# Kernel tuning notes

Hardware: AMD Instinct MI355X
Metric: run time of the kernel (lower is better)

## Reference

```python
import jax, jax.numpy as jnp
import numpy as np

N = 262144   # total atoms across all images
D = 128      # fingerprint (input_dimension)
H = 128      # hidden width (hiddenlayers = (128, 128))
S = 4        # number of unique element symbols (experts)
B = 1024     # number of images (segments)


def setup_inputs() -> dict:
    key = jax.random.key(0)
    ks = jax.random.split(key, 10)
    x = jax.random.normal(ks[0], (N, D), dtype=jnp.float32)
    symbol_ids = jax.random.randint(ks[1], (N,), 0, S, dtype=jnp.int32)
    image_ids = jnp.sort(jax.random.randint(ks[2], (N,), 0, B, dtype=jnp.int32))
    # per-symbol MLP params (xavier-ish scaling)
    W1 = jax.random.normal(ks[3], (S, D, H), dtype=jnp.float32) / np.sqrt(D)
    b1 = jnp.zeros((S, H), dtype=jnp.float32)
    W2 = jax.random.normal(ks[4], (S, H, H), dtype=jnp.float32) / np.sqrt(H)
    b2 = jnp.zeros((S, H), dtype=jnp.float32)
    W3 = jax.random.normal(ks[5], (S, H), dtype=jnp.float32) / np.sqrt(H)
    b3 = jnp.zeros((S,), dtype=jnp.float32)
    # per-symbol affine energy scale/shift
    slope = 1.0 + 0.1 * jax.random.normal(ks[6], (S,), dtype=jnp.float32)
    intercept = 0.1 * jax.random.normal(ks[7], (S,), dtype=jnp.float32)
    return {
        "x": x, "W1": W1, "b1": b1, "W2": W2, "b2": b2, "W3": W3, "b3": b3,
        "slope": slope, "intercept": intercept,
        "symbol_ids": symbol_ids, "image_ids": image_ids,
    }


def reference(x, W1, b1, W2, b2, W3, b3, slope, intercept, symbol_ids, image_ids):
    # Run every atom through every symbol's tiny MLP (S small), then select.
    h = jax.nn.relu(jnp.einsum('nd,sdh->nsh', x, W1) + b1)          # [N,S,H]
    h = jax.nn.relu(jnp.einsum('nsh,shk->nsk', h, W2) + b2)         # [N,S,H]
    e = jnp.einsum('nsh,sh->ns', h, W3) + b3                         # [N,S] atomic energy per expert
    e = slope * e + intercept                                        # per-symbol affine
    e_atom = jnp.take_along_axis(e, symbol_ids[:, None].astype(jnp.int32), axis=1)[:, 0]  # [N] routed
    # per-image energy = sum of atomic energies in that image
    return jax.ops.segment_sum(e_atom, image_ids, num_segments=B)    # [B]
```

## Files before the change

kernel.cpp:

```cpp
#include <hip/hip_runtime.h>
#include <hip/hip_bf16.h>
#include <stdint.h>

typedef _Float16 f16x8 __attribute__((ext_vector_type(8)));
typedef __fp16 hf2 __attribute__((ext_vector_type(2)));
typedef float f32x4 __attribute__((ext_vector_type(4)));
typedef unsigned int u32x4 __attribute__((ext_vector_type(4)));
typedef unsigned int u32x2 __attribute__((ext_vector_type(2)));

#define N_ATOMS 262144
#define NSYM 4
#define NIMG 1024

__global__ void hist_kernel(const int* __restrict__ sym, int* __restrict__ wbh) {
  int b = blockIdx.x;
  int i = b * 256 + threadIdx.x;
  int lane = threadIdx.x & 63, wave = threadIdx.x >> 6;
  __shared__ int wcnt[4][NSYM];
  int s = sym[i];
#pragma unroll
  for (int t = 0; t < NSYM; ++t) {
    unsigned long long m = __ballot(s == t);
    if (lane == 0) wcnt[wave][t] = __popcll(m);
  }
  __syncthreads();
  if (threadIdx.x < NSYM)
    wbh[b * 4 + threadIdx.x] = wcnt[0][threadIdx.x] + wcnt[1][threadIdx.x] +
                               wcnt[2][threadIdx.x] + wcnt[3][threadIdx.x];
}

__global__ void offsets_kernel(const int* __restrict__ wbh, int* __restrict__ bases,
                               int* __restrict__ offs, int* __restrict__ perm) {
  __shared__ int wtot[4][NSYM];
  __shared__ int offsh[NSYM + 1];
  __shared__ int totsh[NSYM];
  int t = threadIdx.x, lane = t & 63, wave = t >> 6;
  int pre[4][NSYM];
  int sum[NSYM] = {0, 0, 0, 0};
#pragma unroll
  for (int k = 0; k < 4; ++k)
#pragma unroll
    for (int s2 = 0; s2 < NSYM; ++s2) {
      pre[k][s2] = sum[s2];
      sum[s2] += wbh[(t * 4 + k) * 4 + s2];
    }
  int inc[NSYM] = {sum[0], sum[1], sum[2], sum[3]};
  for (int d = 1; d < 64; d <<= 1) {
#pragma unroll
    for (int s2 = 0; s2 < NSYM; ++s2) {
      int v = __shfl_up(inc[s2], d);
      if (lane >= d) inc[s2] += v;
    }
  }
  if (lane == 63)
#pragma unroll
    for (int s2 = 0; s2 < NSYM; ++s2) wtot[wave][s2] = inc[s2];
  __syncthreads();
  int wb[NSYM];
#pragma unroll
  for (int s2 = 0; s2 < NSYM; ++s2) {
    wb[s2] = 0;
    for (int w = 0; w < wave; ++w) wb[s2] += wtot[w][s2];
  }
  if (t == 255)
#pragma unroll
    for (int s2 = 0; s2 < NSYM; ++s2) totsh[s2] = wb[s2] + inc[s2];
  __syncthreads();
  if (t == 0) {
    int o = 0;
    offsh[0] = 0; offs[0] = 0;
    for (int s2 = 0; s2 < NSYM; ++s2) {
      o += (totsh[s2] + 255) & ~255;
      offsh[s2 + 1] = o; offs[s2 + 1] = o;
    }
  }
  __syncthreads();
#pragma unroll
  for (int k = 0; k < 4; ++k)
#pragma unroll
    for (int s2 = 0; s2 < NSYM; ++s2)
      bases[(t * 4 + k) * 4 + s2] = offsh[s2] + wb[s2] + (inc[s2] - sum[s2]) + pre[k][s2];
  for (int s2 = 0; s2 < NSYM; ++s2) {
    int lo = offsh[s2] + totsh[s2], hi = offsh[s2 + 1];
    for (int i = lo + t; i < hi; i += 256) perm[i] = -1;
  }
}

__global__ void scatter_kernel(const int* __restrict__ sym, const int* __restrict__ bases,
                               int* __restrict__ perm) {
  int b = blockIdx.x;
  int i = b * 256 + threadIdx.x;
  int lane = threadIdx.x & 63, wave = threadIdx.x >> 6;
  __shared__ int wcnt[4][NSYM];
  int s = sym[i];
  unsigned long long mymask = 0;
#pragma unroll
  for (int t = 0; t < NSYM; ++t) {
    unsigned long long m = __ballot(s == t);
    if (lane == 0) wcnt[wave][t] = __popcll(m);
    if (s == t) mymask = m;
  }
  __syncthreads();
  int off = bases[b * 4 + s];
  for (int w = 0; w < wave; ++w) off += wcnt[w][s];
  off += __popcll(mymask & ((1ull << lane) - 1ull));
  perm[off] = i;
}

__global__ void wconv_kernel(const float* __restrict__ W1, const float* __restrict__ W2,
                             unsigned short* __restrict__ wt) {
  int idx = blockIdx.x * 256 + threadIdx.x;
  int t = idx >> 14;
  int layer = t >> 2, s = t & 3;
  int rem = idx & 16383;
  int h = rem >> 7, u = rem & 127;
  int gs = u >> 3, j = u & 7;
  int d = ((gs ^ (h & 7)) << 3) + j;
  const float* W = layer ? W2 : W1;
  _Float16 hv = (_Float16)W[(s * 128 + d) * 128 + h];
  wt[t * 16384 + h * 128 + u] = __builtin_bit_cast(unsigned short, hv);
}

__global__ __launch_bounds__(512, 2) void mlp_gemm(
    const float* __restrict__ x, const unsigned short* __restrict__ wt,
    const int* __restrict__ perm, const int* __restrict__ offs,
    const float* __restrict__ b1, const float* __restrict__ b2,
    const float* __restrict__ W3, const float* __restrict__ b3,
    const float* __restrict__ slope, const float* __restrict__ intercept,
    float* __restrict__ e_atom) {
  extern __shared__ char lds[];

  int s = blockIdx.x >> 6;
  int kblk = blockIdx.x & 63;
  int base = offs[s];
  int T = (offs[s + 1] - base) >> 8;

  int tid = threadIdx.x;
  int wave = tid >> 6, lane = tid & 63;
  int r0 = lane & 15, chunk = lane >> 4;
  int l32 = lane & 31, half = lane >> 5;
  char* stage = lds + 65536 + wave * 8192;

  const unsigned short* w1p = wt + (size_t)(0 + s) * 16384;
  const unsigned short* w2p = wt + (size_t)(4 + s) * 16384;

#pragma unroll
  for (int it = 0; it < 8; ++it) {
    int gb = it * 512 + wave * 64;
    const unsigned short* src = (gb >= 2048) ? (w2p + (size_t)(gb - 2048 + lane) * 8)
                                             : (w1p + (size_t)(gb + lane) * 8);
    __builtin_amdgcn_global_load_lds((const unsigned int*)src,
                                     (unsigned int*)(lds + (size_t)gb * 16), 16, 0, 0);
  }

  float b1v[8], b2v[8], w3v[8];
#pragma unroll
  for (int cf = 0; cf < 8; ++cf) {
    b1v[cf] = b1[s * 128 + cf * 16 + r0];
    b2v[cf] = b2[s * 128 + cf * 16 + r0];
    w3v[cf] = W3[s * 128 + cf * 16 + r0];
  }
  float sl = slope[s], ic = intercept[s], bb = b3[s];

  int cur_perm = (kblk < T) ? perm[base + (kblk << 8) + wave * 32 + l32] : -1;
  float4 raw[16];
#pragma unroll
  for (int it = 0; it < 16; ++it) {
    int atom = __shfl(cur_perm, it * 2 + half);
    raw[it] = *(const float4*)(x + (size_t)(atom < 0 ? 0 : atom) * 128 + l32 * 4);
  }

  __syncthreads();

  f32x4 zero4 = {0.f, 0.f, 0.f, 0.f};

  for (int t = kblk; t < T; t += 64) {
    int tn = t + 64;
    int nperm = -1;
    if (tn < T) nperm = perm[base + (tn << 8) + wave * 32 + l32];

#pragma unroll
    for (int it = 0; it < 16; ++it) {
      int row = it * 2 + half;
      hf2 p0 = __builtin_amdgcn_cvt_pkrtz(raw[it].x, raw[it].y);
      hf2 p1 = __builtin_amdgcn_cvt_pkrtz(raw[it].z, raw[it].w);
      u32x2 w2 = {__builtin_bit_cast(unsigned int, p0), __builtin_bit_cast(unsigned int, p1)};
      int gs = (l32 >> 1) ^ (row & 7);
      *(u32x2*)(stage + row * 256 + gs * 16 + (l32 & 1) * 8) = w2;
    }
    f16x8 ah[8];
#pragma unroll
    for (int rf = 0; rf < 2; ++rf)
#pragma unroll
      for (int kk = 0; kk < 4; ++kk) {
        int row = rf * 16 + r0;
        ah[rf * 4 + kk] = *(const f16x8*)(stage + row * 256 +
                                          (((kk * 4 + chunk) ^ (row & 7)) << 4));
      }

    f32x4 acc[2][8];
#pragma unroll
    for (int i = 0; i < 2; ++i)
#pragma unroll
      for (int j = 0; j < 8; ++j) acc[i][j] = zero4;

#pragma unroll
    for (int k = 0; k < 4; ++k)
#pragma unroll
      for (int cf = 0; cf < 8; ++cf) {
        int row = cf * 16 + r0;
        f16x8 bh = *(const f16x8*)(lds + row * 256 +
                                   ((((k * 4 + chunk)) << 4) ^ ((row & 7) << 4)));
        acc[0][cf] = __builtin_amdgcn_mfma_f32_16x16x32_f16(ah[k], bh, acc[0][cf], 0, 0, 0);
        acc[1][cf] = __builtin_amdgcn_mfma_f32_16x16x32_f16(ah[4 + k], bh, acc[1][cf], 0, 0, 0);
      }

#pragma unroll
    for (int hp2 = 0; hp2 < 2; ++hp2) {
#pragma unroll
      for (int cf4 = 0; cf4 < 4; ++cf4) {
        int cf = hp2 * 4 + cf4;
        float bias = b1v[cf];
        int colp = cf4 * 16 + r0;
#pragma unroll
        for (int rf = 0; rf < 2; ++rf)
#pragma unroll
          for (int rr = 0; rr < 4; ++rr) {
            int row = rf * 16 + chunk * 4 + rr;
            float v = fmaxf(acc[rf][cf][rr] + bias, 0.f);
            unsigned short h = __builtin_bit_cast(unsigned short, (_Float16)v);
            int cc = colp ^ (chunk << 4) ^ (rr << 2);
            *(unsigned int*)(stage + row * 256 + cc * 4) = ((unsigned int)h << 16) | h;
          }
      }
#pragma unroll
      for (int kk2 = 0; kk2 < 2; ++kk2) {
        int kk = hp2 * 2 + kk2;
#pragma unroll
        for (int rf = 0; rf < 2; ++rf) {
          int row = rf * 16 + r0;
          int xr3 = ((r0 >> 2) << 4) ^ ((r0 & 3) << 2);
          int c0 = kk2 * 32 + chunk * 8;
          u32x4 pa = *(const u32x4*)(stage + row * 256 + (c0 ^ xr3) * 4);
          u32x4 pb = *(const u32x4*)(stage + row * 256 + ((c0 + 4) ^ xr3) * 4);
          unsigned int h01 = (pa[0] >> 16) | (pa[1] & 0xffff0000u);
          unsigned int h23 = (pa[2] >> 16) | (pa[3] & 0xffff0000u);
          unsigned int h45 = (pb[0] >> 16) | (pb[1] & 0xffff0000u);
          unsigned int h67 = (pb[2] >> 16) | (pb[3] & 0xffff0000u);
          u32x4 hq = {h01, h23, h45, h67};
          ah[rf * 4 + kk] = __builtin_bit_cast(f16x8, hq);
        }
      }
    }

    if (tn < T) {
#pragma unroll
      for (int it = 0; it < 16; ++it) {
        int atom = __shfl(nperm, it * 2 + half);
        raw[it] = *(const float4*)(x + (size_t)(atom < 0 ? 0 : atom) * 128 + l32 * 4);
      }
    }

#pragma unroll
    for (int i = 0; i < 2; ++i)
#pragma unroll
      for (int j = 0; j < 8; ++j) acc[i][j] = zero4;

#pragma unroll
    for (int k = 0; k < 4; ++k)
#pragma unroll
      for (int cf = 0; cf < 8; ++cf) {
        int row = cf * 16 + r0;
        f16x8 bh = *(const f16x8*)(lds + 32768 + row * 256 +
                                   ((((k * 4 + chunk)) << 4) ^ ((row & 7) << 4)));
        acc[0][cf] = __builtin_amdgcn_mfma_f32_16x16x32_f16(ah[k], bh, acc[0][cf], 0, 0, 0);
        acc[1][cf] = __builtin_amdgcn_mfma_f32_16x16x32_f16(ah[4 + k], bh, acc[1][cf], 0, 0, 0);
      }

    float p[2][4] = {{0.f, 0.f, 0.f, 0.f}, {0.f, 0.f, 0.f, 0.f}};
#pragma unroll
    for (int cf = 0; cf < 8; ++cf)
#pragma unroll
      for (int rf = 0; rf < 2; ++rf)
#pragma unroll
        for (int rr = 0; rr < 4; ++rr)
          p[rf][rr] += fmaxf(acc[rf][cf][rr] + b2v[cf], 0.f) * w3v[cf];
#pragma unroll
    for (int m = 1; m < 16; m <<= 1)
#pragma unroll
      for (int rf = 0; rf < 2; ++rf)
#pragma unroll
        for (int rr = 0; rr < 4; ++rr) p[rf][rr] += __shfl_xor(p[rf][rr], m);

    int atom_w[2][4];
#pragma unroll
    for (int rf = 0; rf < 2; ++rf)
#pragma unroll
      for (int rr = 0; rr < 4; ++rr)
        atom_w[rf][rr] = __shfl(cur_perm, rf * 16 + chunk * 4 + rr);

    if (r0 == 0) {
#pragma unroll
      for (int rf = 0; rf < 2; ++rf)
#pragma unroll
        for (int rr = 0; rr < 4; ++rr)
          if (atom_w[rf][rr] >= 0)
            e_atom[atom_w[rf][rr]] = sl * (p[rf][rr] + bb) + ic;
    }

    cur_perm = nperm;
  }
}

__global__ void segsum_kernel(const float* __restrict__ e_atom, const int* __restrict__ img,
                              float* __restrict__ out, int n) {
  int b = blockIdx.x;
  int lo = 0, hi = n;
  while (lo < hi) { int m = (lo + hi) >> 1; if (img[m] < b) lo = m + 1; else hi = m; }
  int lo2 = lo, hi2 = n;
  while (lo2 < hi2) { int m = (lo2 + hi2) >> 1; if (img[m] < b + 1) lo2 = m + 1; else hi2 = m; }
  float sum = 0.f;
  for (int i = lo + threadIdx.x; i < lo2; i += blockDim.x) sum += e_atom[i];
  for (int m = 32; m; m >>= 1) sum += __shfl_down(sum, m);
  __shared__ float part[4];
  int lane = threadIdx.x & 63, wave = threadIdx.x >> 6;
  if (lane == 0) part[wave] = sum;
  __syncthreads();
  if (threadIdx.x == 0) out[b] = part[0] + part[1] + part[2] + part[3];
}

extern "C" void kernel_launch(void* const* d_in, const int* in_sizes, int n_in,
                              void* d_out, int out_size, void* d_ws, size_t ws_size,
                              hipStream_t stream) {
  const float* x         = (const float*)d_in[0];
  const float* W1        = (const float*)d_in[1];
  const float* b1        = (const float*)d_in[2];
  const float* W2        = (const float*)d_in[3];
  const float* b2        = (const float*)d_in[4];
  const float* W3        = (const float*)d_in[5];
  const float* b3        = (const float*)d_in[6];
  const float* slope     = (const float*)d_in[7];
  const float* intercept = (const float*)d_in[8];
  const int* sym         = (const int*)d_in[9];
  const int* img         = (const int*)d_in[10];

  char* ws = (char*)d_ws;
  int* wbh    = (int*)ws;
  int* bases  = (int*)(ws + 16384);
  int* offs   = (int*)(ws + 32768);
  int* perm   = (int*)(ws + 32832);
  float* e_atom = (float*)(ws + 32832 + 1052672);
  unsigned short* wt = (unsigned short*)(ws + 2134080);

  hist_kernel<<<1024, 256, 0, stream>>>(sym, wbh);
  offsets_kernel<<<1, 256, 0, stream>>>(wbh, bases, offs, perm);
  scatter_kernel<<<1024, 256, 0, stream>>>(sym, bases, perm);
  wconv_kernel<<<512, 256, 0, stream>>>(W1, W2, wt);
  mlp_gemm<<<256, 512, 131072, stream>>>(x, wt, perm, offs, b1, b2,
                                         W3, b3, slope, intercept, e_atom);
  segsum_kernel<<<NIMG, 256, 0, stream>>>(e_atom, img, (float*)d_out, N_ATOMS);
}
```

Before: 64.89 us.

## Fuse segment sum into MLP via fixed-point atomics and merge prep kernels

The per-image segment sum moves into the MLP epilogue. Each atom energy is converted to 64-bit fixed point and atomically added to its image slot, which removes the e_atom buffer and the binary-search segsum kernel. A small finalize kernel converts the sums back to float. Weight conversion and accumulator zeroing are folded into the offsets launch to cut launch count. The next-tile x prefetch is issued earlier, and MFMA loops get raised wave priority. The cost is atomic contention per image and reduced precision from the fixed-point scale.

```diff
diff --git a/kernel.cpp b/kernel.cpp
--- a/kernel.cpp
+++ b/kernel.cpp
@@ -11,6 +11,7 @@
 #define N_ATOMS 262144
 #define NSYM 4
 #define NIMG 1024
+#define FIXSCALE 1073741824.0f
 
 __global__ void hist_kernel(const int* __restrict__ sym, int* __restrict__ wbh) {
   int b = blockIdx.x;
@@ -29,8 +30,29 @@
                                wcnt[2][threadIdx.x] + wcnt[3][threadIdx.x];
 }
 
-__global__ void offsets_kernel(const int* __restrict__ wbh, int* __restrict__ bases,
-                               int* __restrict__ offs, int* __restrict__ perm) {
+__global__ void fusedprep_kernel(const int* __restrict__ wbh, int* __restrict__ bases,
+                                 int* __restrict__ offs, int* __restrict__ perm,
+                                 const float* __restrict__ W1, const float* __restrict__ W2,
+                                 unsigned short* __restrict__ wt,
+                                 unsigned long long* __restrict__ acc64) {
+  if (blockIdx.x >= 1 && blockIdx.x <= 512) {
+    int idx = (blockIdx.x - 1) * 256 + threadIdx.x;
+    int t = idx >> 14;
+    int layer = t >> 2, s = t & 3;
+    int rem = idx & 16383;
+    int h = rem >> 7, u = rem & 127;
+    int gs = u >> 3, j = u & 7;
+    int d = ((gs ^ (h & 7)) << 3) + j;
+    const float* W = layer ? W2 : W1;
+    _Float16 hv = (_Float16)W[(s * 128 + d) * 128 + h];
+    wt[t * 16384 + h * 128 + u] = __builtin_bit_cast(unsigned short, hv);
+    return;
+  }
+  if (blockIdx.x == 513) {
+#pragma unroll
+    for (int k = 0; k < 4; ++k) acc64[threadIdx.x * 4 + k] = 0ull;
+    return;
+  }
   __shared__ int wtot[4][NSYM];
   __shared__ int offsh[NSYM + 1];
   __shared__ int totsh[NSYM];
@@ -107,27 +129,13 @@
   perm[off] = i;
 }
 
-__global__ void wconv_kernel(const float* __restrict__ W1, const float* __restrict__ W2,
-                             unsigned short* __restrict__ wt) {
-  int idx = blockIdx.x * 256 + threadIdx.x;
-  int t = idx >> 14;
-  int layer = t >> 2, s = t & 3;
-  int rem = idx & 16383;
-  int h = rem >> 7, u = rem & 127;
-  int gs = u >> 3, j = u & 7;
-  int d = ((gs ^ (h & 7)) << 3) + j;
-  const float* W = layer ? W2 : W1;
-  _Float16 hv = (_Float16)W[(s * 128 + d) * 128 + h];
-  wt[t * 16384 + h * 128 + u] = __builtin_bit_cast(unsigned short, hv);
-}
-
 __global__ __launch_bounds__(512, 2) void mlp_gemm(
     const float* __restrict__ x, const unsigned short* __restrict__ wt,
     const int* __restrict__ perm, const int* __restrict__ offs,
     const float* __restrict__ b1, const float* __restrict__ b2,
     const float* __restrict__ W3, const float* __restrict__ b3,
     const float* __restrict__ slope, const float* __restrict__ intercept,
-    float* __restrict__ e_atom) {
+    const int* __restrict__ img, unsigned long long* __restrict__ acc64) {
   extern __shared__ char lds[];
 
   int s = blockIdx.x >> 6;
@@ -198,12 +206,21 @@
                                           (((kk * 4 + chunk) ^ (row & 7)) << 4));
       }
 
+    if (tn < T) {
+#pragma unroll
+      for (int it = 0; it < 16; ++it) {
+        int atom = __shfl(nperm, it * 2 + half);
+        raw[it] = *(const float4*)(x + (size_t)(atom < 0 ? 0 : atom) * 128 + l32 * 4);
+      }
+    }
+
     f32x4 acc[2][8];
 #pragma unroll
     for (int i = 0; i < 2; ++i)
 #pragma unroll
       for (int j = 0; j < 8; ++j) acc[i][j] = zero4;
 
+    __builtin_amdgcn_s_setprio(1);
 #pragma unroll
     for (int k = 0; k < 4; ++k)
 #pragma unroll
@@ -214,6 +231,7 @@
         acc[0][cf] = __builtin_amdgcn_mfma_f32_16x16x32_f16(ah[k], bh, acc[0][cf], 0, 0, 0);
         acc[1][cf] = __builtin_amdgcn_mfma_f32_16x16x32_f16(ah[4 + k], bh, acc[1][cf], 0, 0, 0);
       }
+    __builtin_amdgcn_s_setprio(0);
 
 #pragma unroll
     for (int hp2 = 0; hp2 < 2; ++hp2) {
@@ -253,19 +271,12 @@
       }
     }
 
-    if (tn < T) {
-#pragma unroll
-      for (int it = 0; it < 16; ++it) {
-        int atom = __shfl(nperm, it * 2 + half);
-        raw[it] = *(const float4*)(x + (size_t)(atom < 0 ? 0 : atom) * 128 + l32 * 4);
-      }
-    }
-
 #pragma unroll
     for (int i = 0; i < 2; ++i)
 #pragma unroll
       for (int j = 0; j < 8; ++j) acc[i][j] = zero4;
 
+    __builtin_amdgcn_s_setprio(1);
 #pragma unroll
     for (int k = 0; k < 4; ++k)
 #pragma unroll
@@ -276,6 +287,7 @@
         acc[0][cf] = __builtin_amdgcn_mfma_f32_16x16x32_f16(ah[k], bh, acc[0][cf], 0, 0, 0);
         acc[1][cf] = __builtin_amdgcn_mfma_f32_16x16x32_f16(ah[4 + k], bh, acc[1][cf], 0, 0, 0);
       }
+    __builtin_amdgcn_s_setprio(0);
 
     float p[2][4] = {{0.f, 0.f, 0.f, 0.f}, {0.f, 0.f, 0.f, 0.f}};
 #pragma unroll
@@ -303,30 +315,25 @@
 #pragma unroll
       for (int rf = 0; rf < 2; ++rf)
 #pragma unroll
-        for (int rr = 0; rr < 4; ++rr)
-          if (atom_w[rf][rr] >= 0)
-            e_atom[atom_w[rf][rr]] = sl * (p[rf][rr] + bb) + ic;
+        for (int rr = 0; rr < 4; ++rr) {
+          int a = atom_w[rf][rr];
+          if (a >= 0) {
+            float ev = sl * (p[rf][rr] + bb) + ic;
+            long long q = llrintf(ev * FIXSCALE);
+            atomicAdd(&acc64[img[a]], (unsigned long long)q);
+          }
+        }
     }
 
     cur_perm = nperm;
   }
 }
 
-__global__ void segsum_kernel(const float* __restrict__ e_atom, const int* __restrict__ img,
-                              float* __restrict__ out, int n) {
-  int b = blockIdx.x;
-  int lo = 0, hi = n;
-  while (lo < hi) { int m = (lo + hi) >> 1; if (img[m] < b) lo = m + 1; else hi = m; }
-  int lo2 = lo, hi2 = n;
-  while (lo2 < hi2) { int m = (lo2 + hi2) >> 1; if (img[m] < b + 1) lo2 = m + 1; else hi2 = m; }
-  float sum = 0.f;
-  for (int i = lo + threadIdx.x; i < lo2; i += blockDim.x) sum += e_atom[i];
-  for (int m = 32; m; m >>= 1) sum += __shfl_down(sum, m);
-  __shared__ float part[4];
-  int lane = threadIdx.x & 63, wave = threadIdx.x >> 6;
-  if (lane == 0) part[wave] = sum;
-  __syncthreads();
-  if (threadIdx.x == 0) out[b] = part[0] + part[1] + part[2] + part[3];
+__global__ void finalize_kernel(const unsigned long long* __restrict__ acc64,
+                                float* __restrict__ out) {
+  int b = blockIdx.x * 256 + threadIdx.x;
+  if (b < NIMG)
+    out[b] = (float)((double)(long long)acc64[b] * (1.0 / (double)FIXSCALE));
 }
 
 extern "C" void kernel_launch(void* const* d_in, const int* in_sizes, int n_in,
@@ -349,14 +356,13 @@
   int* bases  = (int*)(ws + 16384);
   int* offs   = (int*)(ws + 32768);
   int* perm   = (int*)(ws + 32832);
-  float* e_atom = (float*)(ws + 32832 + 1052672);
-  unsigned short* wt = (unsigned short*)(ws + 2134080);
+  unsigned long long* acc64 = (unsigned long long*)(ws + 32832 + 1052672);
+  unsigned short* wt = (unsigned short*)(ws + 32832 + 1052672 + 8192);
 
   hist_kernel<<<1024, 256, 0, stream>>>(sym, wbh);
-  offsets_kernel<<<1, 256, 0, stream>>>(wbh, bases, offs, perm);
+  fusedprep_kernel<<<514, 256, 0, stream>>>(wbh, bases, offs, perm, W1, W2, wt, acc64);
   scatter_kernel<<<1024, 256, 0, stream>>>(sym, bases, perm);
-  wconv_kernel<<<512, 256, 0, stream>>>(W1, W2, wt);
   mlp_gemm<<<256, 512, 131072, stream>>>(x, wt, perm, offs, b1, b2,
-                                         W3, b3, slope, intercept, e_atom);
-  segsum_kernel<<<NIMG, 256, 0, stream>>>(e_atom, img, (float*)d_out, N_ATOMS);
-}
+                                         W3, b3, slope, intercept, img, acc64);
+  finalize_kernel<<<4, 256, 0, stream>>>(acc64, (float*)d_out);
+}
```

New measurement: 140.9 us. 117% more time.
